# Optimization experiments

Measured on AMD Instinct MI355X. Metric: run time of the kernel, lower is better.

The kernel has to match this reference:

```python
import jax, jax.numpy as jnp
import numpy as np

NUM_TOKENS = 1048576
NUM_EXPERTS = 64


def setup_inputs() -> dict:
    key = jax.random.key(0)
    router_logits_fp32 = jax.random.normal(key, (NUM_TOKENS, NUM_EXPERTS), dtype=jnp.float32)
    return {"router_logits_fp32": router_logits_fp32, "top_k": 8}


def reference(router_logits_fp32, top_k):
    # Fused softmax over experts + top-k selection (aiter.topk_softmax with renorm=True).
    probs = jax.nn.softmax(router_logits_fp32, axis=-1)          # [T, E]
    topk_weights, topk_ids = jax.lax.top_k(probs, top_k)         # [T, K], [T, K]
    # renormalize selected weights to sum to 1 per token (the trailing True flag)
    topk_weights = topk_weights / jnp.sum(topk_weights, axis=-1, keepdims=True)
    num_tokens = router_logits_fp32.shape[0]
    # token_expert_indices[t, k] = t * top_k + k (row-major source-row mapping used
    # later for the token permutation/scatter into expert buffers)
    token_expert_indices = jnp.arange(num_tokens * top_k, dtype=jnp.int32).reshape(num_tokens, top_k)
    return topk_weights, topk_ids.astype(jnp.int32), token_expert_indices
```

## Files before the change

### kernel.cpp

```cpp
#include <hip/hip_runtime.h>
#include <stdint.h>


typedef float f32x4 __attribute__((ext_vector_type(4)));

#define DPP_QUAD_XOR1   0xB1
#define DPP_QUAD_XOR2   0x4E
#define DPP_HALF_MIRROR 0x141

template<int CTRL>
static __device__ __forceinline__ uint32_t dpp32(uint32_t x) {
    return (uint32_t)__builtin_amdgcn_update_dpp(0, (int)x, CTRL, 0xF, 0xF, true);
}
template<int CTRL>
static __device__ __forceinline__ uint64_t dpp64(uint64_t x) {
    int lo = __builtin_amdgcn_update_dpp(0, (int)(uint32_t)x,         CTRL, 0xF, 0xF, true);
    int hi = __builtin_amdgcn_update_dpp(0, (int)(uint32_t)(x >> 32), CTRL, 0xF, 0xF, true);
    return ((uint64_t)(uint32_t)hi << 32) | (uint32_t)lo;
}
template<int CTRL>
static __device__ __forceinline__ float dppf(float x) {
    int i = __builtin_amdgcn_update_dpp(0, __float_as_int(x), CTRL, 0xF, 0xF, true);
    return __int_as_float(i);
}

#define CE32(x, y) { uint32_t gt_ = (x > y) ? x : y; uint32_t lt_ = (x > y) ? y : x; \
                     x = gt_; y = lt_; }
#define CEU(x, y) { uint64_t a_ = x, b_ = y; bool c_ = a_ < b_; \
                    x = c_ ? b_ : a_; y = c_ ? a_ : b_; }

template<int CTRL>
static __device__ __forceinline__ void merge_u32(uint32_t k[8]) {
    uint32_t m[8];
#pragma unroll
    for (int i = 0; i < 8; ++i) {
        uint32_t p = dpp32<CTRL>(k[7 - i]);
        m[i] = (k[i] > p) ? k[i] : p;
    }
    CE32(m[0], m[4]) CE32(m[1], m[5]) CE32(m[2], m[6]) CE32(m[3], m[7])
    CE32(m[0], m[2]) CE32(m[1], m[3]) CE32(m[4], m[6]) CE32(m[5], m[7])
    CE32(m[0], m[1]) CE32(m[2], m[3]) CE32(m[4], m[5]) CE32(m[6], m[7])
#pragma unroll
    for (int i = 0; i < 8; ++i) k[i] = m[i];
}

static __device__ __forceinline__ uint32_t mono(float v) {
    uint32_t u = __float_as_uint(v);
    return u ^ (uint32_t)(((int32_t)u >> 31) | 0x80000000);
}
static __device__ __forceinline__ float unmono(uint32_t m) {
    uint32_t u = (m & 0x80000000u) ? (m ^ 0x80000000u) : ~m;
    return __uint_as_float(u);
}
static __device__ __forceinline__ uint32_t nzmask(uint32_t d) {
    return (uint32_t)(((int32_t)(d | (0u - d))) >> 31);
}
static __device__ __forceinline__ uint32_t bsel(uint32_t mask, uint32_t b, uint32_t a) {
    return (mask & b) | (~mask & a);
}

__global__ __launch_bounds__(256, 8) void topk_softmax_k(
    const float* __restrict__ logits,
    float* __restrict__ out_w,
    float* __restrict__ out_id,
    float* __restrict__ out_tei,
    int T)
{
    const int  lane = threadIdx.x & 63;
    const int  wv   = (int)(threadIdx.x >> 6);
    const long t0   = (long)blockIdx.x * 32 + (long)wv * 8;
    if (t0 >= T) return;

    const int  sub = lane & 7;
    const bool act = (t0 + (lane >> 3)) < T;

    const f32x4* src = reinterpret_cast<const f32x4*>(logits)
                     + (act ? (t0 * 16 + (long)lane * 2) : 0);
    f32x4 a = __builtin_nontemporal_load(src);
    f32x4 b = __builtin_nontemporal_load(src + 1);

    uint32_t o[8] = { mono(a.x), mono(a.y), mono(a.z), mono(a.w),
                      mono(b.x), mono(b.y), mono(b.z), mono(b.w) };

    uint32_t k[8];
#pragma unroll
    for (int j = 0; j < 8; ++j) k[j] = o[j];

    CE32(k[0],k[1]) CE32(k[2],k[3]) CE32(k[4],k[5]) CE32(k[6],k[7])
    CE32(k[0],k[2]) CE32(k[1],k[3]) CE32(k[4],k[6]) CE32(k[5],k[7])
    CE32(k[1],k[2]) CE32(k[5],k[6])
    CE32(k[0],k[4]) CE32(k[1],k[5]) CE32(k[2],k[6]) CE32(k[3],k[7])
    CE32(k[2],k[4]) CE32(k[3],k[5])
    CE32(k[1],k[2]) CE32(k[3],k[4]) CE32(k[5],k[6])

    merge_u32<DPP_QUAD_XOR1>(k);
    merge_u32<DPP_QUAD_XOR2>(k);
    merge_u32<DPP_HALF_MIRROR>(k);

    uint32_t goodm = 0xFFFFFFFFu;
#pragma unroll
    for (int i = 0; i < 7; ++i) goodm &= nzmask(k[i] ^ k[i + 1]);

    const uint32_t m1 = 0u - (uint32_t)(sub & 1);
    const uint32_t m2 = 0u - (uint32_t)((sub >> 1) & 1);
    const uint32_t m4 = 0u - (uint32_t)((sub >> 2) & 1);
    uint32_t t4a = bsel(m4, k[4], k[0]);
    uint32_t t4b = bsel(m4, k[5], k[1]);
    uint32_t t4c = bsel(m4, k[6], k[2]);
    uint32_t t4d = bsel(m4, k[7], k[3]);
    uint32_t t2a = bsel(m2, t4c, t4a);
    uint32_t t2b = bsel(m2, t4d, t4b);
    uint32_t selmono = bsel(m1, t2b, t2a);
    uint32_t maxmono = k[0];

    const uint32_t idbase = (uint32_t)(sub * 8);
    uint32_t loc = 0xFFFFFFFFu;
#pragma unroll
    for (int j = 0; j < 8; ++j) {
        uint32_t cand = (idbase + (uint32_t)j) | nzmask(o[j] ^ selmono);
        loc = (loc < cand) ? loc : cand;
    }
    { uint32_t p = dpp32<DPP_QUAD_XOR1>(loc);   loc = (loc < p) ? loc : p; }
    { uint32_t p = dpp32<DPP_QUAD_XOR2>(loc);   loc = (loc < p) ? loc : p; }
    { uint32_t p = dpp32<DPP_HALF_MIRROR>(loc); loc = (loc < p) ? loc : p; }
    int idx = (int)loc;

    if (__any(goodm != 0xFFFFFFFFu)) {
        const uint32_t cb = (uint32_t)(63 - sub * 8);
        uint64_t kk[8];
#pragma unroll
        for (int j = 0; j < 8; ++j)
            kk[j] = ((uint64_t)o[j] << 6) | (uint64_t)(cb - (uint32_t)j);

        CEU(kk[0],kk[1]) CEU(kk[2],kk[3]) CEU(kk[4],kk[5]) CEU(kk[6],kk[7])
        CEU(kk[0],kk[2]) CEU(kk[1],kk[3]) CEU(kk[4],kk[6]) CEU(kk[5],kk[7])
        CEU(kk[1],kk[2]) CEU(kk[5],kk[6])
        CEU(kk[0],kk[4]) CEU(kk[1],kk[5]) CEU(kk[2],kk[6]) CEU(kk[3],kk[7])
        CEU(kk[2],kk[4]) CEU(kk[3],kk[5])
        CEU(kk[1],kk[2]) CEU(kk[3],kk[4]) CEU(kk[5],kk[6])

        uint64_t mykey = 0, mtop = 0;
#pragma unroll
        for (int r = 0; r < 8; ++r) {
            uint64_t w = kk[0];
            { uint64_t t = dpp64<DPP_QUAD_XOR1>(w);   if (t > w) w = t; }
            { uint64_t t = dpp64<DPP_QUAD_XOR2>(w);   if (t > w) w = t; }
            { uint64_t t = dpp64<DPP_HALF_MIRROR>(w); if (t > w) w = t; }
            if (r == 0)   mtop  = w;
            if (sub == r) mykey = w;
            bool pop = (kk[0] == w);
            kk[0] = pop ? kk[1] : kk[0];
            kk[1] = pop ? kk[2] : kk[1];
            kk[2] = pop ? kk[3] : kk[2];
            kk[3] = pop ? kk[4] : kk[3];
            kk[4] = pop ? kk[5] : kk[4];
            kk[5] = pop ? kk[6] : kk[5];
            kk[6] = pop ? kk[7] : kk[6];
            kk[7] = pop ? 0     : kk[7];
        }
        selmono = (uint32_t)(mykey >> 6);
        maxmono = (uint32_t)(mtop  >> 6);
        idx = 63 - (int)((uint32_t)mykey & 63u);
    }

    const float v  = unmono(selmono);
    const float mv = unmono(maxmono);
    float e = __expf(v - mv);
    float s = e;
    s += dppf<DPP_QUAD_XOR1>(s);
    s += dppf<DPP_QUAD_XOR2>(s);
    s += dppf<DPP_HALF_MIRROR>(s);
    float wgt = e * __builtin_amdgcn_rcpf(s);

    if (act) {
        const long oi = t0 * 8 + lane;
        __builtin_nontemporal_store(wgt,        &out_w[oi]);
        __builtin_nontemporal_store((float)idx, &out_id[oi]);
        __builtin_nontemporal_store((float)oi,  &out_tei[oi]);
    }
}

extern "C" void kernel_launch(void* const* d_in, const int* in_sizes, int n_in,
                              void* d_out, int out_size, void* d_ws, size_t ws_size,
                              hipStream_t stream) {
    const float* logits = (const float*)d_in[0];
    const int T = in_sizes[0] / 64;

    float* outw = (float*)d_out;
    float* outi = outw + (size_t)T * 8;
    float* outt = outi + (size_t)T * 8;

    const int blocks = (T + 31) / 32;
    hipLaunchKernelGGL(topk_softmax_k, dim3(blocks), dim3(256), 0, stream,
                       logits, outw, outi, outt, T);
}
```

Baseline: 70.05 us.

## Pack expert index into low mantissa bits of sort keys to skip index search

Embeds the expert index in the low 6 bits of each 32-bit monotone key so the fast sorting path yields indices directly, removing the per-lane index search and its DPP min-reduction. Because truncating 6 mantissa bits can reorder near-ties, it adds a count of elements at or above the 8th key and a check for keys equal above the low bits, and falls back to the exact 64-bit path when either fires. The fast path spends a few more ALU ops on the count and its reduction in exchange for dropping the search.

```diff
diff --git a/kernel.cpp b/kernel.cpp
--- a/kernel.cpp
+++ b/kernel.cpp
@@ -52,9 +52,6 @@
     uint32_t u = (m & 0x80000000u) ? (m ^ 0x80000000u) : ~m;
     return __uint_as_float(u);
 }
-static __device__ __forceinline__ uint32_t nzmask(uint32_t d) {
-    return (uint32_t)(((int32_t)(d | (0u - d))) >> 31);
-}
 static __device__ __forceinline__ uint32_t bsel(uint32_t mask, uint32_t b, uint32_t a) {
     return (mask & b) | (~mask & a);
 }
@@ -82,9 +79,11 @@
     uint32_t o[8] = { mono(a.x), mono(a.y), mono(a.z), mono(a.w),
                       mono(b.x), mono(b.y), mono(b.z), mono(b.w) };
 
+    const uint32_t cb = (uint32_t)(63 - sub * 8);
     uint32_t k[8];
 #pragma unroll
-    for (int j = 0; j < 8; ++j) k[j] = o[j];
+    for (int j = 0; j < 8; ++j)
+        k[j] = (o[j] & 0xFFFFFFC0u) | (cb - (uint32_t)j);
 
     CE32(k[0],k[1]) CE32(k[2],k[3]) CE32(k[4],k[5]) CE32(k[6],k[7])
     CE32(k[0],k[2]) CE32(k[1],k[3]) CE32(k[4],k[6]) CE32(k[5],k[7])
@@ -97,9 +96,20 @@
     merge_u32<DPP_QUAD_XOR2>(k);
     merge_u32<DPP_HALF_MIRROR>(k);
 
-    uint32_t goodm = 0xFFFFFFFFu;
+    const uint32_t k7 = k[7];
+    uint32_t qcnt = 0;
 #pragma unroll
-    for (int i = 0; i < 7; ++i) goodm &= nzmask(k[i] ^ k[i + 1]);
+    for (int j = 0; j < 8; ++j)
+        qcnt += ((o[j] | 63u) >= k7) ? 1u : 0u;
+    qcnt += dpp32<DPP_QUAD_XOR1>(qcnt);
+    qcnt += dpp32<DPP_QUAD_XOR2>(qcnt);
+    qcnt += dpp32<DPP_HALF_MIRROR>(qcnt);
+    uint32_t dmin = 0xFFFFFFFFu;
+#pragma unroll
+    for (int i = 0; i < 7; ++i) {
+        uint32_t d = (k[i] ^ k[i + 1]) >> 6;
+        dmin = (d < dmin) ? d : dmin;
+    }
 
     const uint32_t m1 = 0u - (uint32_t)(sub & 1);
     const uint32_t m2 = 0u - (uint32_t)((sub >> 1) & 1);
@@ -110,23 +120,13 @@
     uint32_t t4d = bsel(m4, k[7], k[3]);
     uint32_t t2a = bsel(m2, t4c, t4a);
     uint32_t t2b = bsel(m2, t4d, t4b);
-    uint32_t selmono = bsel(m1, t2b, t2a);
-    uint32_t maxmono = k[0];
+    uint32_t sel = bsel(m1, t2b, t2a);
 
-    const uint32_t idbase = (uint32_t)(sub * 8);
-    uint32_t loc = 0xFFFFFFFFu;
-#pragma unroll
-    for (int j = 0; j < 8; ++j) {
-        uint32_t cand = (idbase + (uint32_t)j) | nzmask(o[j] ^ selmono);
-        loc = (loc < cand) ? loc : cand;
-    }
-    { uint32_t p = dpp32<DPP_QUAD_XOR1>(loc);   loc = (loc < p) ? loc : p; }
-    { uint32_t p = dpp32<DPP_QUAD_XOR2>(loc);   loc = (loc < p) ? loc : p; }
-    { uint32_t p = dpp32<DPP_HALF_MIRROR>(loc); loc = (loc < p) ? loc : p; }
-    int idx = (int)loc;
+    uint32_t selmono = sel  & 0xFFFFFFC0u;
+    uint32_t maxmono = k[0] & 0xFFFFFFC0u;
+    int      idx     = 63 - (int)(sel & 63u);
 
-    if (__any(goodm != 0xFFFFFFFFu)) {
-        const uint32_t cb = (uint32_t)(63 - sub * 8);
+    if (__any((qcnt != 8u) || (dmin == 0u))) {
         uint64_t kk[8];
 #pragma unroll
         for (int j = 0; j < 8; ++j)
```

Measured after the change: 73.43 us. +4.8%, slower.
